# Performance work log

Hardware: AMD Instinct MI355X
Metric: run time of the kernel (lower is better)

## Reference

```python
import jax, jax.numpy as jnp
import numpy as np

B, N_IN, N_OUT, NNZ, IN_C, OUT_C = 2, 50000, 12500, 500000, 256, 256


def setup_inputs() -> dict:
    key = jax.random.key(0)
    k1, k2, k3, k4, k5, k6 = jax.random.split(key, 6)
    x = jax.random.normal(k1, (B, N_IN, IN_C), dtype=jnp.float32)
    rows = jax.random.randint(k2, (NNZ,), 0, N_OUT, dtype=jnp.int32)
    cols = jax.random.randint(k3, (NNZ,), 0, N_IN, dtype=jnp.int32)
    vals = jax.random.uniform(k4, (NNZ,), dtype=jnp.float32)
    weight = jax.random.normal(k5, (IN_C, OUT_C), dtype=jnp.float32) / N_OUT
    bias = jax.random.normal(k6, (N_OUT, OUT_C), dtype=jnp.float32) / N_OUT
    return {"x": x, "rows": rows, "cols": cols, "vals": vals,
            "weight": weight, "bias": bias}


def reference(x, rows, cols, vals, weight, bias):
    # per-batch spmm: (A @ x_b) via gather + segment_sum, then dense projection.
    # Equivalent to the original block-diagonal torch.spmm over the batch.
    def spmm_one(xb):  # xb: [n_in, in_c]
        gathered = xb[cols] * vals[:, None]          # [nnz, in_c]
        return jax.ops.segment_sum(gathered, rows, num_segments=N_OUT)

    ax = jax.vmap(spmm_one)(x)                       # [B, n_out, in_c]
    return jnp.einsum('bni,io->bno', ax, weight) + bias
```

## Files before the change

### kernel.cpp

```cpp
#include <hip/hip_runtime.h>
#include <hip/hip_bf16.h>

typedef unsigned short u16;
typedef unsigned int   u32;
typedef __attribute__((ext_vector_type(8))) short bf16x8;
typedef __attribute__((ext_vector_type(4))) float f32x4;

constexpr int B_    = 2;
constexpr int N_IN  = 50000;
constexpr int N_OUT = 12500;
constexpr int NNZ   = 500000;
constexpr int C     = 256;
constexpr int M_TOT = B_ * N_OUT;

constexpr int QB     = N_IN / 8;
constexpr int NB_H   = 128;
constexpr int EPB    = (NNZ + NB_H - 1) / NB_H;
constexpr int NSLICE = (N_OUT + 255) / 256;

__device__ __forceinline__ u16 f2b(float f) {
    __hip_bfloat16 h = __float2bfloat16(f);
    return *(u16*)&h;
}

__device__ __forceinline__ u32 pack4(float4 f, float inv) {
    u32 u0 = (u32)(int)(rintf(f.x * inv) + 128.f);
    u32 u1 = (u32)(int)(rintf(f.y * inv) + 128.f);
    u32 u2 = (u32)(int)(rintf(f.z * inv) + 128.f);
    u32 u3 = (u32)(int)(rintf(f.w * inv) + 128.f);
    return u0 | (u1 << 8) | (u2 << 16) | (u3 << 24);
}

__global__ __launch_bounds__(256) void quant_hist_k(const float* __restrict__ x,
                                                    u32* __restrict__ xq,
                                                    float* __restrict__ xs,
                                                    const int* __restrict__ rows,
                                                    u16* __restrict__ partial) {
    __shared__ u32 lc[N_OUT];
    int blk = blockIdx.x;
    int t   = threadIdx.x;
    if (blk < QB) {
        int wv  = t >> 6, l = t & 63;
        int rec = l >> 4;
        int j   = l & 15;
        int n   = blk * 8 + wv * 2 + (rec >> 1);
        int b   = rec & 1;
        const float4* px = (const float4*)(x + ((size_t)b * N_IN + n) * C + j * 16);
        float4 f0 = px[0], f1 = px[1], f2 = px[2], f3 = px[3];
        float m0 = fmaxf(fmaxf(fabsf(f0.x), fabsf(f0.y)), fmaxf(fabsf(f0.z), fabsf(f0.w)));
        float m1 = fmaxf(fmaxf(fabsf(f1.x), fabsf(f1.y)), fmaxf(fabsf(f1.z), fabsf(f1.w)));
        float m2 = fmaxf(fmaxf(fabsf(f2.x), fabsf(f2.y)), fmaxf(fabsf(f2.z), fabsf(f2.w)));
        float m3 = fmaxf(fmaxf(fabsf(f3.x), fabsf(f3.y)), fmaxf(fabsf(f3.z), fabsf(f3.w)));
        float m  = fmaxf(fmaxf(m0, m1), fmaxf(m2, m3));
#pragma unroll
        for (int off = 1; off < 16; off <<= 1)
            m = fmaxf(m, __shfl_xor(m, off, 64));
        float qstep = m * (1.f / 127.f);
        float inv   = 127.f / m;
        if (j == 0) xs[n * 2 + b] = qstep;
        uint4 pk;
        pk.x = pack4(f0, inv);
        pk.y = pack4(f1, inv);
        pk.z = pack4(f2, inv);
        pk.w = pack4(f3, inv);
        *(uint4*)(xq + (size_t)n * 128 + b * 64 + j * 4) = pk;
    } else {
        int hb = blk - QB;
        for (int i = t; i < N_OUT; i += 256) lc[i] = 0;
        __syncthreads();
        int base = hb * EPB;
        int end  = base + EPB < NNZ ? base + EPB : NNZ;
        for (int i = base + t; i < end; i += 256)
            atomicAdd(&lc[rows[i]], 1u);
        __syncthreads();
        for (int i = t; i < N_OUT; i += 256)
            partial[(size_t)hb * N_OUT + i] = (u16)lc[i];
    }
}

__global__ __launch_bounds__(256) void binpre2_k(const u16* __restrict__ partial,
                                                 u16* __restrict__ bp,
                                                 u32* __restrict__ startlocal,
                                                 int* __restrict__ slicesum) {
    int blk = blockIdx.x;
    int bin = blk * 256 + threadIdx.x;
    u32 run = 0;
    if (bin < N_OUT) {
        for (int b = 0; b < NB_H; ++b) {
            u32 c = partial[(size_t)b * N_OUT + bin];
            bp[(size_t)b * N_OUT + bin] = (u16)run;
            run += c;
        }
    }
    int lane = threadIdx.x & 63, wv = threadIdx.x >> 6;
    u32 v = run;
#pragma unroll
    for (int off = 1; off < 64; off <<= 1) {
        u32 t2 = __shfl_up(v, off, 64);
        if (lane >= off) v += t2;
    }
    __shared__ u32 wsum[4];
    if (lane == 63) wsum[wv] = v;
    __syncthreads();
    u32 woff = 0;
    for (int w = 0; w < wv; ++w) woff += wsum[w];
    u32 incl = woff + v;
    if (bin < N_OUT) startlocal[bin] = incl - run;
    if (threadIdx.x == 255) slicesum[blk] = (int)incl;
}

__global__ __launch_bounds__(256) void sliceoff_tw_k(const int* __restrict__ slicesum,
                                                     int* __restrict__ sliceoff,
                                                     const float* __restrict__ w,
                                                     u16* __restrict__ wt) {
    int tid = threadIdx.x;
    if (blockIdx.x > 0) {
        int n = blockIdx.x - 1;
        wt[(size_t)n * C + tid] = f2b(w[(size_t)tid * C + n]);
        return;
    }
    if (tid < 64) {
        int s = (tid < NSLICE) ? slicesum[tid] : 0;
        int v = s;
#pragma unroll
        for (int off = 1; off < 64; off <<= 1) {
            int t2 = __shfl_up(v, off, 64);
            if (tid >= off) v += t2;
        }
        if (tid < NSLICE) sliceoff[tid] = v - s;
    }
}

__global__ __launch_bounds__(256) void scatter_k(const int* __restrict__ rows,
                                                 const int* __restrict__ cols,
                                                 const float* __restrict__ vals,
                                                 const int* __restrict__ sliceoff,
                                                 const u32* __restrict__ startlocal,
                                                 const u16* __restrict__ bp,
                                                 int2* __restrict__ edges) {
    __shared__ u32 lc[N_OUT];
    int t = threadIdx.x, blk = blockIdx.x;
    for (int i = t; i < N_OUT; i += 256)
        lc[i] = (u32)sliceoff[i >> 8] + startlocal[i] + (u32)bp[(size_t)blk * N_OUT + i];
    __syncthreads();
    int base = blk * EPB;
    int end  = base + EPB < NNZ ? base + EPB : NNZ;
    for (int i = base + t; i < end; i += 256) {
        int r = rows[i];
        u32 p = atomicAdd(&lc[r], 1u);
        edges[p] = make_int2(cols[i], __float_as_int(vals[i]));
    }
}

__global__ __launch_bounds__(256) void spmm_q_k(const u32* __restrict__ xq,
                                                const float* __restrict__ xs,
                                                const int* __restrict__ sliceoff,
                                                const u32* __restrict__ startlocal,
                                                const int2* __restrict__ edges,
                                                u32* __restrict__ ax) {
    int r    = blockIdx.x;
    int wv   = threadIdx.x >> 6;
    int lane = threadIdx.x & 63;
    int b    = lane >> 5;
    int g    = lane & 31;
    int loff = b * 64 + g * 2;

    int e0 = sliceoff[r >> 8] + (int)startlocal[r];
    int e1 = (r == N_OUT - 1) ? NNZ : sliceoff[(r + 1) >> 8] + (int)startlocal[r + 1];

    float acc[8];
#pragma unroll
    for (int j = 0; j < 8; ++j) acc[j] = 0.f;
    float S = 0.f;

    auto body = [&](int2 d) {
        float vs = __int_as_float(d.y) * xs[d.x * 2 + b];
        uint2 q  = *(const uint2*)(xq + (size_t)d.x * 128 + loff);
        S += vs;
        acc[0] += vs * (float)( q.x        & 255u);
        acc[1] += vs * (float)((q.x >>  8) & 255u);
        acc[2] += vs * (float)((q.x >> 16) & 255u);
        acc[3] += vs * (float)( q.x >> 24        );
        acc[4] += vs * (float)( q.y        & 255u);
        acc[5] += vs * (float)((q.y >>  8) & 255u);
        acc[6] += vs * (float)((q.y >> 16) & 255u);
        acc[7] += vs * (float)( q.y >> 24        );
    };

    int e = e0 + wv;
    for (; e + 12 < e1; e += 16) {
        int2 d0 = edges[e], d1 = edges[e + 4], d2 = edges[e + 8], d3 = edges[e + 12];
        body(d0); body(d1); body(d2); body(d3);
    }
    for (; e < e1; e += 4) body(edges[e]);

    __shared__ float red[4][64][8];
#pragma unroll
    for (int j = 0; j < 8; ++j) red[wv][lane][j] = acc[j] - 128.f * S;
    __syncthreads();
    if (wv == 0) {
        float4 lo = *(float4*)&red[0][lane][0];
        float4 hi = *(float4*)&red[0][lane][4];
#pragma unroll
        for (int ww = 1; ww < 4; ++ww) {
            float4 l2 = *(float4*)&red[ww][lane][0];
            float4 h2 = *(float4*)&red[ww][lane][4];
            lo.x += l2.x; lo.y += l2.y; lo.z += l2.z; lo.w += l2.w;
            hi.x += h2.x; hi.y += h2.y; hi.z += h2.z; hi.w += h2.w;
        }
        uint4 pk;
        pk.x = (u32)f2b(lo.x) | ((u32)f2b(lo.y) << 16);
        pk.y = (u32)f2b(lo.z) | ((u32)f2b(lo.w) << 16);
        pk.z = (u32)f2b(hi.x) | ((u32)f2b(hi.y) << 16);
        pk.w = (u32)f2b(hi.z) | ((u32)f2b(hi.w) << 16);
        u32* axrow = ax + ((size_t)b * N_OUT + r) * (C / 2);
        *(uint4*)(axrow + g * 4) = pk;
    }
}

__global__ __launch_bounds__(256) void gemm_k(const u32* __restrict__ ax,
                                              const u16* __restrict__ wt,
                                              const float* __restrict__ bias,
                                              float* __restrict__ out) {
    int wave = threadIdx.x >> 6;
    int lane = threadIdx.x & 63;
    int quad = lane >> 4;
    int l15  = lane & 15;
    int m0   = blockIdx.x * 16;
    int n0   = wave * 64;

    int mrow = m0 + l15;
    int mr_c = mrow < M_TOT ? mrow : (M_TOT - 1);
    const u16* arow = (const u16*)(ax + (size_t)mr_c * (C / 2));

    f32x4 acc[4];
#pragma unroll
    for (int t = 0; t < 4; ++t) acc[t] = (f32x4){0.f, 0.f, 0.f, 0.f};

#pragma unroll
    for (int kt = 0; kt < 8; ++kt) {
        int k0 = kt * 32 + quad * 8;
        bf16x8 afrag = *(const bf16x8*)(arow + k0);
#pragma unroll
        for (int nt = 0; nt < 4; ++nt) {
            bf16x8 bfrag = *(const bf16x8*)(wt + (size_t)(n0 + nt * 16 + l15) * C + k0);
            acc[nt] = __builtin_amdgcn_mfma_f32_16x16x32_bf16(afrag, bfrag, acc[nt], 0, 0, 0);
        }
    }

#pragma unroll
    for (int nt = 0; nt < 4; ++nt) {
        int col = n0 + nt * 16 + l15;
#pragma unroll
        for (int reg = 0; reg < 4; ++reg) {
            int rg = m0 + quad * 4 + reg;
            if (rg < M_TOT) {
                int rloc = (rg >= N_OUT) ? rg - N_OUT : rg;
                out[(size_t)rg * C + col] = acc[nt][reg] + bias[(size_t)rloc * C + col];
            }
        }
    }
}

extern "C" void kernel_launch(void* const* d_in, const int* in_sizes, int n_in,
                              void* d_out, int out_size, void* d_ws, size_t ws_size,
                              hipStream_t stream) {
    const float* x      = (const float*)d_in[0];
    const int*   rows   = (const int*)d_in[1];
    const int*   cols   = (const int*)d_in[2];
    const float* vals   = (const float*)d_in[3];
    const float* weight = (const float*)d_in[4];
    const float* bias   = (const float*)d_in[5];
    float*       out    = (float*)d_out;

    char*  ws  = (char*)d_ws;
    size_t off = 0;
    auto alloc = [&](size_t bytes) -> void* {
        void* p = ws + off;
        off = (off + bytes + 255) & ~(size_t)255;
        return p;
    };
    u32*   startlocal = (u32*) alloc((size_t)N_OUT * 4);
    int*   slicesum   = (int*) alloc((size_t)NSLICE * 4);
    int*   sliceoff   = (int*) alloc((size_t)NSLICE * 4);
    int2*  edges      = (int2*)alloc((size_t)NNZ * 8);
    u32*   ax         = (u32*) alloc((size_t)M_TOT * (C / 2) * 4);
    u16*   wt         = (u16*) alloc((size_t)C * C * 2);
    u32*   xq         = (u32*) alloc((size_t)N_IN * 128 * 4);
    float* xs         = (float*)alloc((size_t)N_IN * B_ * 4);
    if (off > ws_size) return;

    u16* partial = (u16*)ax;
    u16* bp      = partial + (size_t)NB_H * N_OUT;

    quant_hist_k <<<QB + NB_H, 256, 0, stream>>>(x, xq, xs, rows, partial);
    binpre2_k    <<<NSLICE, 256, 0, stream>>>(partial, bp, startlocal, slicesum);
    sliceoff_tw_k<<<1 + C, 256, 0, stream>>>(slicesum, sliceoff, weight, wt);
    scatter_k    <<<NB_H, 256, 0, stream>>>(rows, cols, vals, sliceoff, startlocal, bp, edges);
    spmm_q_k     <<<N_OUT, 256, 0, stream>>>(xq, xs, sliceoff, startlocal, edges, ax);
    gemm_k       <<<(M_TOT + 15) / 16, 256, 0, stream>>>(ax, wt, bias, out);
}
```

Baseline: 308.1 us.

## Fold slice-offset scan into scatter, merge weight transpose, widen spmm gathers

The weight transpose moves into the quantize/histogram kernel, and the slice-offset prefix scan moves into each scatter block. This drops one kernel launch. Scatter also writes a flat row-start array, so spmm reads two values instead of computing offsets. In spmm each lane now loads 16 bytes of quantized x per edge, covering both batches, and two edges are processed per wave, with a cross-half shuffle reduction before the shared-memory reduction. The cost is redundant scans in every scatter block and more accumulator registers per thread.

```diff
diff --git a/kernel.cpp b/kernel.cpp
--- a/kernel.cpp
+++ b/kernel.cpp
@@ -31,11 +31,13 @@
     return u0 | (u1 << 8) | (u2 << 16) | (u3 << 24);
 }
 
-__global__ __launch_bounds__(256) void quant_hist_k(const float* __restrict__ x,
-                                                    u32* __restrict__ xq,
-                                                    float* __restrict__ xs,
-                                                    const int* __restrict__ rows,
-                                                    u16* __restrict__ partial) {
+__global__ __launch_bounds__(256) void quant_hist_tw_k(const float* __restrict__ x,
+                                                       u32* __restrict__ xq,
+                                                       float* __restrict__ xs,
+                                                       const int* __restrict__ rows,
+                                                       u16* __restrict__ partial,
+                                                       const float* __restrict__ w,
+                                                       u16* __restrict__ wt) {
     __shared__ u32 lc[N_OUT];
     int blk = blockIdx.x;
     int t   = threadIdx.x;
@@ -64,7 +66,7 @@
         pk.z = pack4(f2, inv);
         pk.w = pack4(f3, inv);
         *(uint4*)(xq + (size_t)n * 128 + b * 64 + j * 4) = pk;
-    } else {
+    } else if (blk < QB + NB_H) {
         int hb = blk - QB;
         for (int i = t; i < N_OUT; i += 256) lc[i] = 0;
         __syncthreads();
@@ -75,6 +77,9 @@
         __syncthreads();
         for (int i = t; i < N_OUT; i += 256)
             partial[(size_t)hb * N_OUT + i] = (u16)lc[i];
+    } else {
+        int n = blk - QB - NB_H;
+        wt[(size_t)n * C + t] = f2b(w[(size_t)t * C + n]);
     }
 }
 
@@ -109,39 +114,34 @@
     if (threadIdx.x == 255) slicesum[blk] = (int)incl;
 }
 
-__global__ __launch_bounds__(256) void sliceoff_tw_k(const int* __restrict__ slicesum,
-                                                     int* __restrict__ sliceoff,
-                                                     const float* __restrict__ w,
-                                                     u16* __restrict__ wt) {
-    int tid = threadIdx.x;
-    if (blockIdx.x > 0) {
-        int n = blockIdx.x - 1;
-        wt[(size_t)n * C + tid] = f2b(w[(size_t)tid * C + n]);
-        return;
-    }
-    if (tid < 64) {
-        int s = (tid < NSLICE) ? slicesum[tid] : 0;
-        int v = s;
-#pragma unroll
-        for (int off = 1; off < 64; off <<= 1) {
-            int t2 = __shfl_up(v, off, 64);
-            if (tid >= off) v += t2;
-        }
-        if (tid < NSLICE) sliceoff[tid] = v - s;
-    }
-}
-
 __global__ __launch_bounds__(256) void scatter_k(const int* __restrict__ rows,
                                                  const int* __restrict__ cols,
                                                  const float* __restrict__ vals,
-                                                 const int* __restrict__ sliceoff,
+                                                 const int* __restrict__ slicesum,
                                                  const u32* __restrict__ startlocal,
                                                  const u16* __restrict__ bp,
-                                                 int2* __restrict__ edges) {
+                                                 int2* __restrict__ edges,
+                                                 int* __restrict__ start) {
     __shared__ u32 lc[N_OUT];
+    __shared__ int soff[64];
     int t = threadIdx.x, blk = blockIdx.x;
-    for (int i = t; i < N_OUT; i += 256)
-        lc[i] = (u32)sliceoff[i >> 8] + startlocal[i] + (u32)bp[(size_t)blk * N_OUT + i];
+    if (t < 64) {
+        int s = (t < NSLICE) ? slicesum[t] : 0;
+        int v = s;
+#pragma unroll
+        for (int off = 1; off < 64; off <<= 1) {
+            int t2 = __shfl_up(v, off, 64);
+            if (t >= off) v += t2;
+        }
+        soff[t] = v - s;
+    }
+    __syncthreads();
+    for (int i = t; i < N_OUT; i += 256) {
+        u32 st = (u32)soff[i >> 8] + startlocal[i];
+        lc[i] = st + (u32)bp[(size_t)blk * N_OUT + i];
+        if (blk == 0) start[i] = (int)st;
+    }
+    if (blk == 0 && t == 0) start[N_OUT] = NNZ;
     __syncthreads();
     int base = blk * EPB;
     int end  = base + EPB < NNZ ? base + EPB : NNZ;
@@ -154,66 +154,82 @@
 
 __global__ __launch_bounds__(256) void spmm_q_k(const u32* __restrict__ xq,
                                                 const float* __restrict__ xs,
-                                                const int* __restrict__ sliceoff,
-                                                const u32* __restrict__ startlocal,
+                                                const int* __restrict__ start,
                                                 const int2* __restrict__ edges,
                                                 u32* __restrict__ ax) {
     int r    = blockIdx.x;
     int wv   = threadIdx.x >> 6;
     int lane = threadIdx.x & 63;
-    int b    = lane >> 5;
-    int g    = lane & 31;
-    int loff = b * 64 + g * 2;
-
-    int e0 = sliceoff[r >> 8] + (int)startlocal[r];
-    int e1 = (r == N_OUT - 1) ? NNZ : sliceoff[(r + 1) >> 8] + (int)startlocal[r + 1];
-
-    float acc[8];
-#pragma unroll
-    for (int j = 0; j < 8; ++j) acc[j] = 0.f;
+    int h    = lane >> 5;
+    int g2   = lane & 31;
+    int b    = g2 >> 4;
+
+    int e0 = start[r], e1 = start[r + 1];
+
+    float acc[16];
+#pragma unroll
+    for (int j = 0; j < 16; ++j) acc[j] = 0.f;
     float S = 0.f;
 
     auto body = [&](int2 d) {
         float vs = __int_as_float(d.y) * xs[d.x * 2 + b];
-        uint2 q  = *(const uint2*)(xq + (size_t)d.x * 128 + loff);
+        uint4 q  = *(const uint4*)(xq + (size_t)d.x * 128 + g2 * 4);
         S += vs;
-        acc[0] += vs * (float)( q.x        & 255u);
-        acc[1] += vs * (float)((q.x >>  8) & 255u);
-        acc[2] += vs * (float)((q.x >> 16) & 255u);
-        acc[3] += vs * (float)( q.x >> 24        );
-        acc[4] += vs * (float)( q.y        & 255u);
-        acc[5] += vs * (float)((q.y >>  8) & 255u);
-        acc[6] += vs * (float)((q.y >> 16) & 255u);
-        acc[7] += vs * (float)( q.y >> 24        );
+        acc[ 0] += vs * (float)( q.x        & 255u);
+        acc[ 1] += vs * (float)((q.x >>  8) & 255u);
+        acc[ 2] += vs * (float)((q.x >> 16) & 255u);
+        acc[ 3] += vs * (float)( q.x >> 24        );
+        acc[ 4] += vs * (float)( q.y        & 255u);
+        acc[ 5] += vs * (float)((q.y >>  8) & 255u);
+        acc[ 6] += vs * (float)((q.y >> 16) & 255u);
+        acc[ 7] += vs * (float)( q.y >> 24        );
+        acc[ 8] += vs * (float)( q.z        & 255u);
+        acc[ 9] += vs * (float)((q.z >>  8) & 255u);
+        acc[10] += vs * (float)((q.z >> 16) & 255u);
+        acc[11] += vs * (float)( q.z >> 24        );
+        acc[12] += vs * (float)( q.w        & 255u);
+        acc[13] += vs * (float)((q.w >>  8) & 255u);
+        acc[14] += vs * (float)((q.w >> 16) & 255u);
+        acc[15] += vs * (float)( q.w >> 24        );
     };
 
-    int e = e0 + wv;
-    for (; e + 12 < e1; e += 16) {
-        int2 d0 = edges[e], d1 = edges[e + 4], d2 = edges[e + 8], d3 = edges[e + 12];
-        body(d0); body(d1); body(d2); body(d3);
-    }
-    for (; e < e1; e += 4) body(edges[e]);
-
-    __shared__ float red[4][64][8];
-#pragma unroll
-    for (int j = 0; j < 8; ++j) red[wv][lane][j] = acc[j] - 128.f * S;
+    int e = e0 + wv * 2 + h;
+    for (; e + 8 < e1; e += 16) {
+        int2 d0 = edges[e], d1 = edges[e + 8];
+        body(d0); body(d1);
+    }
+    for (; e < e1; e += 8) body(edges[e]);
+
+#pragma unroll
+    for (int j = 0; j < 16; ++j) acc[j] += __shfl_xor(acc[j], 32, 64);
+    S += __shfl_xor(S, 32, 64);
+
+    __shared__ float red[4][32][20];
+    if (h == 0) {
+#pragma unroll
+        for (int j = 0; j < 16; ++j) red[wv][g2][j] = acc[j] - 128.f * S;
+    }
     __syncthreads();
     if (wv == 0) {
-        float4 lo = *(float4*)&red[0][lane][0];
-        float4 hi = *(float4*)&red[0][lane][4];
-#pragma unroll
-        for (int ww = 1; ww < 4; ++ww) {
-            float4 l2 = *(float4*)&red[ww][lane][0];
-            float4 h2 = *(float4*)&red[ww][lane][4];
-            lo.x += l2.x; lo.y += l2.y; lo.z += l2.z; lo.w += l2.w;
-            hi.x += h2.x; hi.y += h2.y; hi.z += h2.z; hi.w += h2.w;
+        int bb  = lane >> 5, g = lane & 31;
+        int idx = bb * 16 + (g >> 1);
+        int j0  = (g & 1) * 8;
+        float o[8];
+#pragma unroll
+        for (int i = 0; i < 8; ++i) o[i] = 0.f;
+#pragma unroll
+        for (int w = 0; w < 4; ++w) {
+            float4 lo = *(float4*)&red[w][idx][j0];
+            float4 hi = *(float4*)&red[w][idx][j0 + 4];
+            o[0] += lo.x; o[1] += lo.y; o[2] += lo.z; o[3] += lo.w;
+            o[4] += hi.x; o[5] += hi.y; o[6] += hi.z; o[7] += hi.w;
         }
         uint4 pk;
-        pk.x = (u32)f2b(lo.x) | ((u32)f2b(lo.y) << 16);
-        pk.y = (u32)f2b(lo.z) | ((u32)f2b(lo.w) << 16);
-        pk.z = (u32)f2b(hi.x) | ((u32)f2b(hi.y) << 16);
-        pk.w = (u32)f2b(hi.z) | ((u32)f2b(hi.w) << 16);
-        u32* axrow = ax + ((size_t)b * N_OUT + r) * (C / 2);
+        pk.x = (u32)f2b(o[0]) | ((u32)f2b(o[1]) << 16);
+        pk.y = (u32)f2b(o[2]) | ((u32)f2b(o[3]) << 16);
+        pk.z = (u32)f2b(o[4]) | ((u32)f2b(o[5]) << 16);
+        pk.w = (u32)f2b(o[6]) | ((u32)f2b(o[7]) << 16);
+        u32* axrow = ax + ((size_t)bb * N_OUT + r) * (C / 2);
         *(uint4*)(axrow + g * 4) = pk;
     }
 }
@@ -282,7 +298,7 @@
     };
     u32*   startlocal = (u32*) alloc((size_t)N_OUT * 4);
     int*   slicesum   = (int*) alloc((size_t)NSLICE * 4);
-    int*   sliceoff   = (int*) alloc((size_t)NSLICE * 4);
+    int*   start      = (int*) alloc((size_t)(N_OUT + 1) * 4);
     int2*  edges      = (int2*)alloc((size_t)NNZ * 8);
     u32*   ax         = (u32*) alloc((size_t)M_TOT * (C / 2) * 4);
     u16*   wt         = (u16*) alloc((size_t)C * C * 2);
@@ -293,10 +309,10 @@
     u16* partial = (u16*)ax;
     u16* bp      = partial + (size_t)NB_H * N_OUT;
 
-    quant_hist_k <<<QB + NB_H, 256, 0, stream>>>(x, xq, xs, rows, partial);
-    binpre2_k    <<<NSLICE, 256, 0, stream>>>(partial, bp, startlocal, slicesum);
-    sliceoff_tw_k<<<1 + C, 256, 0, stream>>>(slicesum, sliceoff, weight, wt);
-    scatter_k    <<<NB_H, 256, 0, stream>>>(rows, cols, vals, sliceoff, startlocal, bp, edges);
-    spmm_q_k     <<<N_OUT, 256, 0, stream>>>(xq, xs, sliceoff, startlocal, edges, ax);
-    gemm_k       <<<(M_TOT + 15) / 16, 256, 0, stream>>>(ax, wt, bias, out);
-}
+    quant_hist_tw_k<<<QB + NB_H + C, 256, 0, stream>>>(x, xq, xs, rows, partial, weight, wt);
+    binpre2_k      <<<NSLICE, 256, 0, stream>>>(partial, bp, startlocal, slicesum);
+    scatter_k      <<<NB_H, 256, 0, stream>>>(rows, cols, vals, slicesum, startlocal, bp,
+                                              edges, start);
+    spmm_q_k       <<<N_OUT, 256, 0, stream>>>(xq, xs, start, edges, ax);
+    gemm_k         <<<(M_TOT + 15) / 16, 256, 0, stream>>>(ax, wt, bias, out);
+}
```

After: 303.2 us. No clear change (-1.6%).
